# Kernel optimization log

Hardware: AMD Instinct MI355X
Metric: run time of the kernel (lower is better)

The kernel has to match this reference:

```python
import jax, jax.numpy as jnp
import numpy as np

# Polynomial coefficients from the original module (hard-coded in forward).
P00, P10, P20, P30 = 0.0, 0.0, 0.0, 0.0      # identity-kernel branch (all zero)
P01, P11, P21 = -0.000287, 0.266, -0.1097    # learned-weight branch
STRIDE, PAD = 1, 1


def _conv(x, w):
    # NCHW input, OIHW kernel -> NCHW output. Equivalent to
    # unfold(x).T @ w.view(O,-1).T reshaped back, i.e. torch's im2col matmul.
    return jax.lax.conv_general_dilated(
        x, w,
        window_strides=(STRIDE, STRIDE),
        padding=[(PAD, PAD), (PAD, PAD)],
        dimension_numbers=('NCHW', 'OIHW', 'NCHW'))


def setup_inputs() -> dict:
    key = jax.random.key(0)
    k1, k2 = jax.random.split(key)
    img = jax.random.normal(k1, (16, 64, 128, 128), dtype=jnp.float32)
    # weights initialized N(0, 0.8) in the original module
    weights = jax.random.normal(k2, (64, 64, 3, 3), dtype=jnp.float32) * 0.8
    identity_kernel = jnp.ones((64, 64, 3, 3), dtype=jnp.float32)
    return {"img": img, "weights": weights, "identity_kernel": identity_kernel}


def reference(img, weights, identity_kernel):
    kh, kw = weights.shape[2], weights.shape[3]
    # Elementwise polynomial applied to the input, then contracted against
    # the (identity, learned) kernels. matmul-with-unfold == convolution,
    # so we express it as two convs instead of materializing im2col.
    poly_id = P00 + P10 * img + P20 * img**2 + P30 * img**3  # == zeros here
    poly_w = P01 + P11 * img + P21 * img**2
    out = _conv(poly_id, identity_kernel) + _conv(poly_w, weights)
    return out / (3 * kh * kw)
```

## Files before the change

kernel.cpp:

```cpp
#include <hip/hip_runtime.h>


typedef __bf16 bf16;
typedef __attribute__((ext_vector_type(8))) __bf16 bf16x8;
typedef __attribute__((ext_vector_type(16))) float f32x16;

static constexpr float A0 = -0.000287f / 27.0f;
static constexpr float A1 =  0.266f    / 27.0f;
static constexpr float A2 = -0.1097f   / 27.0f;

#define NN 16
#define CI 64
#define HH 128
#define WW 128
#define OO 64

__global__ void repack_w(const float* __restrict__ w, bf16* __restrict__ wrb) {
    int idx = blockIdx.x * 256 + threadIdx.x;
    if (idx >= 9 * 8 * 64 * 8) return;
    int cj    = idx & 7;
    int o     = (idx >> 3) & 63;
    int cc8   = (idx >> 9) & 7;
    int slice = idx >> 12;
    int ky = slice / 3, kx = slice - ky * 3;
    int c = cc8 * 8 + cj;
    wrb[idx] = (bf16)w[((o * CI + c) * 3 + ky) * 3 + kx];
}

__global__ __launch_bounds__(512, 4) void conv_mfma(const float* __restrict__ img,
                                                    const bf16* __restrict__ wrb,
                                                    float* __restrict__ out) {
    __shared__ __align__(16) char smem[49920];
    bf16*  ilds = (bf16*)smem;
    float* elds = (float*)smem;

    const int tid = threadIdx.x;
    const int b   = blockIdx.x;
    const int y0  = (b & 31) * 4;
    const int n   = b >> 5;

    const int wv   = tid >> 6;
    const int lane = tid & 63;
    const int lm   = lane & 31;
    const int half = lane >> 5;
    const int yl   = wv >> 1;
    const int Xh   = (wv & 1) * 64;

    auto stage = [&](int chunk, int buf) {
        const int cbase = chunk * 16;
        bf16* dst = ilds + buf * 12480;
        for (int t = tid; t < 780; t += 512) {
            int r   = t / 130;
            int rem = t - r * 130;
            int ccl = rem / 65;
            int xh  = rem - ccl * 65;
            int yi  = y0 - 1 + r;
            bf16* rowp = dst + (r * 2 + ccl) * (130 * 8);
            if (xh < 64) {
                bf16x8 pk0, pk1;
                if ((unsigned)yi < 128u) {
                    const float* p = img + ((n * CI + cbase + ccl * 8) * HH + yi) * WW + 2 * xh;
                    #pragma unroll
                    for (int j = 0; j < 8; ++j) {
                        float2 v = *(const float2*)(p + j * HH * WW);
                        pk0[j] = (bf16)(A0 + v.x * (A1 + A2 * v.x));
                        pk1[j] = (bf16)(A0 + v.y * (A1 + A2 * v.y));
                    }
                } else {
                    #pragma unroll
                    for (int j = 0; j < 8; ++j) { pk0[j] = (bf16)0.0f; pk1[j] = (bf16)0.0f; }
                }
                *(bf16x8*)(rowp + (2 * xh + 1) * 8) = pk0;
                *(bf16x8*)(rowp + (2 * xh + 2) * 8) = pk1;
            } else {
                bf16x8 z;
                #pragma unroll
                for (int j = 0; j < 8; ++j) z[j] = (bf16)0.0f;
                *(bf16x8*)(rowp + 0) = z;
                *(bf16x8*)(rowp + 129 * 8) = z;
            }
        }
    };

    f32x16 acc[2][2];
    #pragma unroll
    for (int i = 0; i < 2; ++i)
        #pragma unroll
        for (int j = 0; j < 2; ++j)
            #pragma unroll
            for (int k = 0; k < 16; ++k) acc[i][j][k] = 0.0f;

    const bf16x8* wfr = (const bf16x8*)wrb;

    stage(0, 0);

    for (int chunk = 0; chunk < 4; ++chunk) {
        __syncthreads();
        if (chunk < 3) stage(chunk + 1, (chunk + 1) & 1);
        const bf16x8* ifr = (const bf16x8*)(ilds + (chunk & 1) * 12480);
        const int cc8g = chunk * 2 + half;
        #pragma unroll
        for (int ky = 0; ky < 3; ++ky) {
            const int r = yl + ky;
            #pragma unroll
            for (int kx = 0; kx < 3; ++kx) {
                const int slice = ky * 3 + kx;
                bf16x8 a0 = wfr[(slice * 8 + cc8g) * 64 + lm];
                bf16x8 a1 = wfr[(slice * 8 + cc8g) * 64 + 32 + lm];
                const int ib = (r * 2 + half) * 130 + Xh + lm + kx;
                bf16x8 b0 = ifr[ib];
                bf16x8 b1 = ifr[ib + 32];
                acc[0][0] = __builtin_amdgcn_mfma_f32_32x32x16_bf16(a0, b0, acc[0][0], 0, 0, 0);
                acc[0][1] = __builtin_amdgcn_mfma_f32_32x32x16_bf16(a0, b1, acc[0][1], 0, 0, 0);
                acc[1][0] = __builtin_amdgcn_mfma_f32_32x32x16_bf16(a1, b0, acc[1][0], 0, 0, 0);
                acc[1][1] = __builtin_amdgcn_mfma_f32_32x32x16_bf16(a1, b1, acc[1][1], 0, 0, 0);
            }
        }
    }

    #pragma unroll
    for (int p = 0; p < 4; ++p) {
        const int ot  = p >> 1;
        const int sub = p & 1;
        __syncthreads();
        #pragma unroll
        for (int xt = 0; xt < 2; ++xt) {
            const int x = Xh + xt * 32 + lm;
            #pragma unroll
            for (int q = 0; q < 2; ++q) {
                #pragma unroll
                for (int rb = 0; rb < 4; ++rb) {
                    const int rg  = (sub * 2 + q) * 4 + rb;
                    const int o16 = rb + 8 * q + 4 * half;
                    elds[(o16 * 4 + yl) * 128 + x] = acc[ot][xt][rg];
                }
            }
        }
        __syncthreads();
        #pragma unroll
        for (int j = 0; j < 4; ++j) {
            const int idx = tid + j * 512;
            const int x4  = idx & 31;
            const int yy  = (idx >> 5) & 3;
            const int o16 = idx >> 7;
            float4 v = ((const float4*)elds)[idx];
            float* dstp = out + ((n * OO + p * 16 + o16) * HH + (y0 + yy)) * WW + x4 * 4;
            *(float4*)dstp = v;
        }
    }
}

extern "C" void kernel_launch(void* const* d_in, const int* in_sizes, int n_in,
                              void* d_out, int out_size, void* d_ws, size_t ws_size,
                              hipStream_t stream) {
    const float* img = (const float*)d_in[0];
    const float* w   = (const float*)d_in[1];
    float* out = (float*)d_out;
    bf16* wrb  = (bf16*)d_ws;

    repack_w<<<(9 * 8 * 64 * 8 + 255) / 256, 256, 0, stream>>>(w, wrb);
    conv_mfma<<<NN * (HH / 4), 512, 0, stream>>>(img, wrb, out);
}
```

Baseline: 134.3 us.

## Halve conv tile width, double grid, and prefetch input into registers across MFMA

Each block now covers 64 output columns instead of 128, which doubles the grid to 1024 blocks and halves per-wave accumulators. Staging is split into a global load into registers issued before the MFMA loop and a bf16 convert-and-write to LDS issued after it, so global latency overlaps compute. Loads are now float4, and the epilogue writes all 64 output channels in a single LDS pass instead of four. The cost is extra halo reads at the column split and fewer MFMAs per LDS fetch, since each B fragment feeds two MFMAs instead of four.

```diff
diff --git a/kernel.cpp b/kernel.cpp
--- a/kernel.cpp
+++ b/kernel.cpp
@@ -2,6 +2,7 @@
 
 
 typedef __bf16 bf16;
+typedef __attribute__((ext_vector_type(4))) __bf16 bf16x4;
 typedef __attribute__((ext_vector_type(8))) __bf16 bf16x8;
 typedef __attribute__((ext_vector_type(16))) float f32x16;
 
@@ -30,123 +31,143 @@
 __global__ __launch_bounds__(512, 4) void conv_mfma(const float* __restrict__ img,
                                                     const bf16* __restrict__ wrb,
                                                     float* __restrict__ out) {
-    __shared__ __align__(16) char smem[49920];
+    __shared__ __align__(16) char smem[65536];
     bf16*  ilds = (bf16*)smem;
     float* elds = (float*)smem;
 
     const int tid = threadIdx.x;
     const int b   = blockIdx.x;
-    const int y0  = (b & 31) * 4;
-    const int n   = b >> 5;
+    const int X0  = (b & 1) * 64;
+    const int y0  = ((b >> 1) & 31) * 4;
+    const int n   = b >> 6;
 
     const int wv   = tid >> 6;
     const int lane = tid & 63;
     const int lm   = lane & 31;
     const int half = lane >> 5;
     const int yl   = wv >> 1;
-    const int Xh   = (wv & 1) * 64;
+    const int xw   = (wv & 1) * 32;
 
-    auto stage = [&](int chunk, int buf) {
-        const int cbase = chunk * 16;
-        bf16* dst = ilds + buf * 12480;
-        for (int t = tid; t < 780; t += 512) {
-            int r   = t / 130;
-            int rem = t - r * 130;
-            int ccl = rem / 65;
-            int xh  = rem - ccl * 65;
-            int yi  = y0 - 1 + r;
-            bf16* rowp = dst + (r * 2 + ccl) * (130 * 8);
-            if (xh < 64) {
-                bf16x8 pk0, pk1;
-                if ((unsigned)yi < 128u) {
-                    const float* p = img + ((n * CI + cbase + ccl * 8) * HH + yi) * WW + 2 * xh;
-                    #pragma unroll
-                    for (int j = 0; j < 8; ++j) {
-                        float2 v = *(const float2*)(p + j * HH * WW);
-                        pk0[j] = (bf16)(A0 + v.x * (A1 + A2 * v.x));
-                        pk1[j] = (bf16)(A0 + v.y * (A1 + A2 * v.y));
-                    }
-                } else {
-                    #pragma unroll
-                    for (int j = 0; j < 8; ++j) { pk0[j] = (bf16)0.0f; pk1[j] = (bf16)0.0f; }
-                }
-                *(bf16x8*)(rowp + (2 * xh + 1) * 8) = pk0;
-                *(bf16x8*)(rowp + (2 * xh + 2) * 8) = pk1;
-            } else {
-                bf16x8 z;
+    auto stage_load = [&](int chunk, float4* v) {
+        if (tid >= 408) return;
+        const int c4  = (tid >= 204) ? 1 : 0;
+        const int id  = tid - 204 * c4;
+        const int r   = id / 34;
+        const int rem = id - r * 34;
+        const int ccl = rem / 17;
+        const int xs  = rem - ccl * 17;
+        const int yi  = y0 - 1 + r;
+        const bool yok = (unsigned)yi < 128u;
+        const int cb  = chunk * 16 + ccl * 8 + c4 * 4;
+        const float* p = img + ((n * CI + cb) * HH + yi) * WW;
+        if (xs < 16) {
+            if (yok) {
                 #pragma unroll
-                for (int j = 0; j < 8; ++j) z[j] = (bf16)0.0f;
-                *(bf16x8*)(rowp + 0) = z;
-                *(bf16x8*)(rowp + 129 * 8) = z;
+                for (int j = 0; j < 4; ++j)
+                    v[j] = *(const float4*)(p + j * HH * WW + X0 + 4 * xs);
+            }
+        } else {
+            #pragma unroll
+            for (int j = 0; j < 4; ++j) { v[j].x = 0.0f; v[j].y = 0.0f; }
+            if (yok && X0 == 64) {
+                #pragma unroll
+                for (int j = 0; j < 4; ++j) v[j].x = p[j * HH * WW + 63];
+            }
+            if (yok && X0 == 0) {
+                #pragma unroll
+                for (int j = 0; j < 4; ++j) v[j].y = p[j * HH * WW + 64];
             }
         }
     };
 
-    f32x16 acc[2][2];
+    auto stage_write = [&](int buf, float4* v) {
+        if (tid >= 408) return;
+        const int c4  = (tid >= 204) ? 1 : 0;
+        const int id  = tid - 204 * c4;
+        const int r   = id / 34;
+        const int rem = id - r * 34;
+        const int ccl = rem / 17;
+        const int xs  = rem - ccl * 17;
+        const int yi  = y0 - 1 + r;
+        const bool yok = (unsigned)yi < 128u;
+        bf16* rowp = ilds + buf * 6336 + ((r * 2 + ccl) * 66) * 8 + c4 * 4;
+        if (xs < 16) {
+            #pragma unroll
+            for (int c = 0; c < 4; ++c) {
+                bf16x4 pk;
+                #pragma unroll
+                for (int j = 0; j < 4; ++j) {
+                    const float x = (c == 0) ? v[j].x : (c == 1) ? v[j].y
+                                   : (c == 2) ? v[j].z : v[j].w;
+                    pk[j] = yok ? (bf16)(A0 + x * (A1 + A2 * x)) : (bf16)0.0f;
+                }
+                *(bf16x4*)(rowp + (4 * xs + 1 + c) * 8) = pk;
+            }
+        } else {
+            bf16x4 pl, pr;
+            const bool lok = yok && (X0 == 64);
+            const bool rok = yok && (X0 == 0);
+            #pragma unroll
+            for (int j = 0; j < 4; ++j) {
+                const float xl = v[j].x, xr = v[j].y;
+                pl[j] = lok ? (bf16)(A0 + xl * (A1 + A2 * xl)) : (bf16)0.0f;
+                pr[j] = rok ? (bf16)(A0 + xr * (A1 + A2 * xr)) : (bf16)0.0f;
+            }
+            *(bf16x4*)(rowp + 0 * 8)  = pl;
+            *(bf16x4*)(rowp + 65 * 8) = pr;
+        }
+    };
+
+    f32x16 acc[2];
     #pragma unroll
-    for (int i = 0; i < 2; ++i)
-        #pragma unroll
-        for (int j = 0; j < 2; ++j)
-            #pragma unroll
-            for (int k = 0; k < 16; ++k) acc[i][j][k] = 0.0f;
+    for (int k = 0; k < 16; ++k) { acc[0][k] = 0.0f; acc[1][k] = 0.0f; }
 
     const bf16x8* wfr = (const bf16x8*)wrb;
 
-    stage(0, 0);
+    float4 v[4];
+    stage_load(0, v);
+    stage_write(0, v);
 
     for (int chunk = 0; chunk < 4; ++chunk) {
         __syncthreads();
-        if (chunk < 3) stage(chunk + 1, (chunk + 1) & 1);
-        const bf16x8* ifr = (const bf16x8*)(ilds + (chunk & 1) * 12480);
+        if (chunk < 3) stage_load(chunk + 1, v);
+        const bf16x8* ifr = (const bf16x8*)(ilds + (chunk & 1) * 6336);
         const int cc8g = chunk * 2 + half;
         #pragma unroll
         for (int ky = 0; ky < 3; ++ky) {
-            const int r = yl + ky;
+            const int rr2 = (yl + ky) * 2 + half;
             #pragma unroll
             for (int kx = 0; kx < 3; ++kx) {
                 const int slice = ky * 3 + kx;
                 bf16x8 a0 = wfr[(slice * 8 + cc8g) * 64 + lm];
                 bf16x8 a1 = wfr[(slice * 8 + cc8g) * 64 + 32 + lm];
-                const int ib = (r * 2 + half) * 130 + Xh + lm + kx;
-                bf16x8 b0 = ifr[ib];
-                bf16x8 b1 = ifr[ib + 32];
-                acc[0][0] = __builtin_amdgcn_mfma_f32_32x32x16_bf16(a0, b0, acc[0][0], 0, 0, 0);
-                acc[0][1] = __builtin_amdgcn_mfma_f32_32x32x16_bf16(a0, b1, acc[0][1], 0, 0, 0);
-                acc[1][0] = __builtin_amdgcn_mfma_f32_32x32x16_bf16(a1, b0, acc[1][0], 0, 0, 0);
-                acc[1][1] = __builtin_amdgcn_mfma_f32_32x32x16_bf16(a1, b1, acc[1][1], 0, 0, 0);
+                bf16x8 b0 = ifr[rr2 * 66 + xw + lm + kx];
+                acc[0] = __builtin_amdgcn_mfma_f32_32x32x16_bf16(a0, b0, acc[0], 0, 0, 0);
+                acc[1] = __builtin_amdgcn_mfma_f32_32x32x16_bf16(a1, b0, acc[1], 0, 0, 0);
             }
         }
+        if (chunk < 3) stage_write((chunk + 1) & 1, v);
     }
 
+    __syncthreads();
     #pragma unroll
-    for (int p = 0; p < 4; ++p) {
-        const int ot  = p >> 1;
-        const int sub = p & 1;
-        __syncthreads();
+    for (int i = 0; i < 2; ++i) {
         #pragma unroll
-        for (int xt = 0; xt < 2; ++xt) {
-            const int x = Xh + xt * 32 + lm;
-            #pragma unroll
-            for (int q = 0; q < 2; ++q) {
-                #pragma unroll
-                for (int rb = 0; rb < 4; ++rb) {
-                    const int rg  = (sub * 2 + q) * 4 + rb;
-                    const int o16 = rb + 8 * q + 4 * half;
-                    elds[(o16 * 4 + yl) * 128 + x] = acc[ot][xt][rg];
-                }
-            }
+        for (int rg = 0; rg < 16; ++rg) {
+            const int o64 = (rg & 3) + 8 * (rg >> 2) + 4 * half + 32 * i;
+            elds[(o64 * 4 + yl) * 64 + xw + lm] = acc[i][rg];
         }
-        __syncthreads();
-        #pragma unroll
-        for (int j = 0; j < 4; ++j) {
-            const int idx = tid + j * 512;
-            const int x4  = idx & 31;
-            const int yy  = (idx >> 5) & 3;
-            const int o16 = idx >> 7;
-            float4 v = ((const float4*)elds)[idx];
-            float* dstp = out + ((n * OO + p * 16 + o16) * HH + (y0 + yy)) * WW + x4 * 4;
-            *(float4*)dstp = v;
-        }
+    }
+    __syncthreads();
+    #pragma unroll
+    for (int j = 0; j < 8; ++j) {
+        const int idx = tid + j * 512;
+        const int x4  = idx & 15;
+        const int yy  = (idx >> 4) & 3;
+        const int o   = idx >> 6;
+        float4 vv = ((const float4*)elds)[idx];
+        float* dstp = out + ((n * OO + o) * HH + (y0 + yy)) * WW + X0 + x4 * 4;
+        *(float4*)dstp = vv;
     }
 }
 
@@ -159,5 +180,5 @@
     bf16* wrb  = (bf16*)d_ws;
 
     repack_w<<<(9 * 8 * 64 * 8 + 255) / 256, 256, 0, stream>>>(w, wrb);
-    conv_mfma<<<NN * (HH / 4), 512, 0, stream>>>(img, wrb, out);
+    conv_mfma<<<NN * (HH / 4) * 2, 512, 0, stream>>>(img, wrb, out);
 }
```

Measured after the change: 145.9 us. 8.6% more time.

## Stage raw input via direct global-to-LDS loads and store outputs directly

Applied to the files above, without the earlier changes.

Replaces per-thread global loads plus in-register polynomial transform with asynchronous global_load_lds DMA of raw fp32 rows into LDS, followed by an LDS-side transform into a single bf16 buffer. Channel-chunk order is staggered across blocks, and the LDS-staged epilogue is replaced with direct scalar global stores from the accumulators. This aims to overlap input fetch with MFMA work and remove epilogue synchronisation. In exchange it uses more LDS (74KB dynamic), which may cut occupancy, and makes the output stores less coalesced.

```diff
diff --git a/kernel.cpp b/kernel.cpp
--- a/kernel.cpp
+++ b/kernel.cpp
@@ -14,6 +14,7 @@
 #define HH 128
 #define WW 128
 #define OO 64
+#define LDS_BYTES 74112
 
 __global__ void repack_w(const float* __restrict__ w, bf16* __restrict__ wrb) {
     int idx = blockIdx.x * 256 + threadIdx.x;
@@ -30,9 +31,9 @@
 __global__ __launch_bounds__(512, 4) void conv_mfma(const float* __restrict__ img,
                                                     const bf16* __restrict__ wrb,
                                                     float* __restrict__ out) {
-    __shared__ __align__(16) char smem[49920];
-    bf16*  ilds = (bf16*)smem;
-    float* elds = (float*)smem;
+    extern __shared__ __align__(16) char smem[];
+    float* raw  = (float*)smem;
+    bf16*  ilds = (bf16*)(smem + 49152);
 
     const int tid = threadIdx.x;
     const int b   = blockIdx.x;
@@ -46,23 +47,37 @@
     const int yl   = wv >> 1;
     const int Xh   = (wv & 1) * 64;
 
-    auto stage = [&](int chunk, int buf) {
-        const int cbase = chunk * 16;
-        bf16* dst = ilds + buf * 12480;
+    auto dma = [&](int chunk) {
+        const int ch = 2 * wv + half;
+        const int x0 = (lane & 31) * 4;
+        #pragma unroll
+        for (int i = 0; i < 6; ++i) {
+            const int yi = y0 - 1 + i;
+            if ((unsigned)yi < 128u) {
+                const float* g = img + ((n * CI + chunk * 16 + ch) * HH + yi) * WW + x0;
+                __builtin_amdgcn_global_load_lds(
+                    (const __attribute__((address_space(1))) void*)g,
+                    (__attribute__((address_space(3))) void*)(raw + (wv + 8 * i) * 256),
+                    16, 0, 0);
+            }
+        }
+    };
+
+    auto transform = [&]() {
         for (int t = tid; t < 780; t += 512) {
             int r   = t / 130;
             int rem = t - r * 130;
             int ccl = rem / 65;
             int xh  = rem - ccl * 65;
             int yi  = y0 - 1 + r;
-            bf16* rowp = dst + (r * 2 + ccl) * (130 * 8);
+            bf16* rowp = ilds + (r * 2 + ccl) * (130 * 8);
             if (xh < 64) {
                 bf16x8 pk0, pk1;
                 if ((unsigned)yi < 128u) {
-                    const float* p = img + ((n * CI + cbase + ccl * 8) * HH + yi) * WW + 2 * xh;
+                    const float* p = raw + (r * 16 + ccl * 8) * 128 + 2 * xh;
                     #pragma unroll
                     for (int j = 0; j < 8; ++j) {
-                        float2 v = *(const float2*)(p + j * HH * WW);
+                        float2 v = *(const float2*)(p + j * 128);
                         pk0[j] = (bf16)(A0 + v.x * (A1 + A2 * v.x));
                         pk1[j] = (bf16)(A0 + v.y * (A1 + A2 * v.y));
                     }
@@ -91,14 +106,19 @@
             for (int k = 0; k < 16; ++k) acc[i][j][k] = 0.0f;
 
     const bf16x8* wfr = (const bf16x8*)wrb;
+    const bf16x8* ifr = (const bf16x8*)ilds;
 
-    stage(0, 0);
+    const int corder = ((b >> 8) & 1) * 2;
 
-    for (int chunk = 0; chunk < 4; ++chunk) {
+    dma(corder);
+    __syncthreads();
+
+    for (int j = 0; j < 4; ++j) {
+        const int cc = (corder + j) & 3;
+        transform();
         __syncthreads();
-        if (chunk < 3) stage(chunk + 1, (chunk + 1) & 1);
-        const bf16x8* ifr = (const bf16x8*)(ilds + (chunk & 1) * 12480);
-        const int cc8g = chunk * 2 + half;
+        if (j < 3) dma((corder + j + 1) & 3);
+        const int cc8g = cc * 2 + half;
         #pragma unroll
         for (int ky = 0; ky < 3; ++ky) {
             const int r = yl + ky;
@@ -116,38 +136,21 @@
                 acc[1][1] = __builtin_amdgcn_mfma_f32_32x32x16_bf16(a1, b1, acc[1][1], 0, 0, 0);
             }
         }
+        if (j < 3) __syncthreads();
     }
 
+    const int ybase = (n * OO * HH + (y0 + yl)) * WW;
     #pragma unroll
-    for (int p = 0; p < 4; ++p) {
-        const int ot  = p >> 1;
-        const int sub = p & 1;
-        __syncthreads();
+    for (int p = 0; p < 2; ++p)
         #pragma unroll
         for (int xt = 0; xt < 2; ++xt) {
             const int x = Xh + xt * 32 + lm;
             #pragma unroll
-            for (int q = 0; q < 2; ++q) {
-                #pragma unroll
-                for (int rb = 0; rb < 4; ++rb) {
-                    const int rg  = (sub * 2 + q) * 4 + rb;
-                    const int o16 = rb + 8 * q + 4 * half;
-                    elds[(o16 * 4 + yl) * 128 + x] = acc[ot][xt][rg];
-                }
+            for (int rg = 0; rg < 16; ++rg) {
+                const int o = (rg & 3) + 8 * (rg >> 2) + 4 * half + 32 * p;
+                out[ybase + o * (HH * WW) + x] = acc[p][xt][rg];
             }
         }
-        __syncthreads();
-        #pragma unroll
-        for (int j = 0; j < 4; ++j) {
-            const int idx = tid + j * 512;
-            const int x4  = idx & 31;
-            const int yy  = (idx >> 5) & 3;
-            const int o16 = idx >> 7;
-            float4 v = ((const float4*)elds)[idx];
-            float* dstp = out + ((n * OO + p * 16 + o16) * HH + (y0 + yy)) * WW + x4 * 4;
-            *(float4*)dstp = v;
-        }
-    }
 }
 
 extern "C" void kernel_launch(void* const* d_in, const int* in_sizes, int n_in,
@@ -158,6 +161,13 @@
     float* out = (float*)d_out;
     bf16* wrb  = (bf16*)d_ws;
 
+    static bool attr_done = false;
+    if (!attr_done) {
+        (void)hipFuncSetAttribute((const void*)conv_mfma,
+                                  hipFuncAttributeMaxDynamicSharedMemorySize, LDS_BYTES);
+        attr_done = true;
+    }
+
     repack_w<<<(9 * 8 * 64 * 8 + 255) / 256, 256, 0, stream>>>(w, wrb);
-    conv_mfma<<<NN * (HH / 4), 512, 0, stream>>>(img, wrb, out);
+    conv_mfma<<<NN * (HH / 4), 512, LDS_BYTES, stream>>>(img, wrb, out);
 }
```

Result: faster. 128.3 us (-4.5%).
